# Kernel optimization log

Hardware: AMD Instinct MI355X
Metric: run time of the kernel (lower is better)

## Reference

```python
import jax, jax.numpy as jnp
import numpy as np

B, T, D, U = 64, 512, 1024, 128


def setup_inputs() -> dict:
    key = jax.random.key(0)
    k1, k2, k3, k4, k5 = jax.random.split(key, 5)
    x = jax.random.normal(k1, (B, T, D), dtype=jnp.float32)
    mask = jnp.ones((B, T), dtype=jnp.int32)
    # learned parameters (glorot-ish scale for kernel)
    kernel = jax.random.normal(k2, (D, U), dtype=jnp.float32) * (1.0 / np.sqrt(D))
    bias = jnp.zeros((U,), dtype=jnp.float32)
    left_boundary = jax.random.normal(k3, (U,), dtype=jnp.float32) * 0.1
    right_boundary = jax.random.normal(k4, (U,), dtype=jnp.float32) * 0.1
    return {"x": x, "mask": mask, "kernel": kernel, "bias": bias,
            "left_boundary": left_boundary, "right_boundary": right_boundary}


def _shift_right(m):  # [B,T,1] -> pad one zero step at front along time
    return jnp.concatenate([jnp.zeros_like(m[:, :1]), m[:, :-1]], axis=1)


def _shift_left(m):  # [B,T,1] -> pad one zero step at end along time
    return jnp.concatenate([m[:, 1:], jnp.zeros_like(m[:, :1])], axis=1)


def reference(x, mask, kernel, bias, left_boundary, right_boundary):
    # input energy: linear activation of dense projection  [B,T,U]
    energy = jnp.einsum('btd,du->btu', x, kernel) + bias
    # boundary energies with mask (faithful to source semantics)
    m = mask.astype(energy.dtype)[:, :, None]                     # [B,T,1]
    start_mask = (m > _shift_right(m)).astype(energy.dtype)       # first valid step
    end_mask = (_shift_left(m) > m).astype(energy.dtype)          # as written in source
    energy = energy + start_mask * left_boundary[None, None, :]
    energy = energy + end_mask * right_boundary[None, None, :]
    return energy
```

## Files before the change

kernel.cpp:

```cpp
#include <hip/hip_runtime.h>

#define TT 512
#define DD 1024
#define UU 128
#define MM 32768
#define BK 64
#define NCHUNK 16

typedef short short8 __attribute__((ext_vector_type(8)));
typedef float f32x4 __attribute__((ext_vector_type(4)));

__device__ __forceinline__ unsigned short f2bf(float f) {
    union { float f; unsigned u; } v; v.f = f;
    unsigned u = v.u;
    return (unsigned short)((u + 0x7fffu + ((u >> 16) & 1u)) >> 16);
}

__device__ __forceinline__ void glds16(const void* g, void* l) {
    __builtin_amdgcn_global_load_lds(
        (const __attribute__((address_space(1))) void*)g,
        (__attribute__((address_space(3))) void*)l, 16, 0, 0);
}

__global__ __launch_bounds__(256) void wprep_kernel(const float* __restrict__ w,
                                                    unsigned short* __restrict__ wt) {
    int tg = blockIdx.x * 256 + threadIdx.x;
    int kg = tg & 7;
    int n  = (tg >> 3) & 127;
    int kc = tg >> 10;
    union { unsigned short s[8]; uint4 v; } o;
#pragma unroll
    for (int j = 0; j < 8; ++j) {
        int k = kc * 64 + kg * 8 + j;
        o.s[j] = f2bf(w[k * 128 + n]);
    }
    *(uint4*)(wt + tg * 8) = o.v;
}

__global__ __launch_bounds__(256, 4) void crf_energy_kernel(
    const float* __restrict__ x,
    const int* __restrict__ mask,
    const unsigned short* __restrict__ wt,
    const float* __restrict__ bias,
    const float* __restrict__ lb,
    const float* __restrict__ rb,
    float* __restrict__ out)
{
    __shared__ float lAf[32 * 64];
    __shared__ unsigned short lBs[128 * 64];

    const int tid  = threadIdx.x;
    const int w    = tid >> 6;
    const int lane = tid & 63;
    const int q    = lane >> 4;
    const int r    = lane & 15;

    const int mt   = w >> 1;
    const int nh   = w & 1;
    const int row0 = blockIdx.x * 32;

    int a_m[2], a_g[2];
#pragma unroll
    for (int j = 0; j < 2; ++j) {
        a_m[j] = w * 8 + j * 4 + (lane >> 4);
        a_g[j] = (lane & 15) ^ (a_m[j] & 15);
    }
    int b_n[4], b_g[4];
#pragma unroll
    for (int j = 0; j < 4; ++j) {
        b_n[j] = w * 32 + j * 8 + (lane >> 3);
        b_g[j] = (lane & 7) ^ (b_n[j] & 7);
    }
    char* const lA_base = (char*)lAf + w * 2048;
    char* const lB_base = (char*)lBs + w * 4096;

    f32x4 acc[4];
#pragma unroll
    for (int nt = 0; nt < 4; ++nt) acc[nt] = (f32x4){0.f, 0.f, 0.f, 0.f};

    for (int kc = 0; kc < NCHUNK; ++kc) {
#pragma unroll
        for (int j = 0; j < 2; ++j)
            glds16(x + (size_t)(row0 + a_m[j]) * DD + kc * BK + a_g[j] * 4,
                   lA_base + j * 1024);
#pragma unroll
        for (int j = 0; j < 4; ++j)
            glds16(wt + (size_t)kc * 8192 + b_n[j] * 64 + b_g[j] * 8,
                   lB_base + j * 1024);
        __syncthreads();

#pragma unroll
        for (int ks = 0; ks < 2; ++ks) {
            const int m  = mt * 16 + r;
            const int g0 = ks * 8 + q * 2;
            const float4 lo = *(const float4*)(&lAf[m * 64 + ((g0     ^ (m & 15)) * 4)]);
            const float4 hi = *(const float4*)(&lAf[m * 64 + (((g0+1) ^ (m & 15)) * 4)]);
            union { unsigned short s[8]; short8 v; } pk;
            pk.s[0] = f2bf(lo.x); pk.s[1] = f2bf(lo.y);
            pk.s[2] = f2bf(lo.z); pk.s[3] = f2bf(lo.w);
            pk.s[4] = f2bf(hi.x); pk.s[5] = f2bf(hi.y);
            pk.s[6] = f2bf(hi.z); pk.s[7] = f2bf(hi.w);
            const short8 a = pk.v;

            short8 b[4];
            const int gb = ks * 4 + q;
#pragma unroll
            for (int nt = 0; nt < 4; ++nt) {
                const int n = nh * 64 + nt * 16 + r;
                b[nt] = *(const short8*)(&lBs[n * 64 + ((gb ^ (n & 7)) * 8)]);
            }
#pragma unroll
            for (int nt = 0; nt < 4; ++nt)
                acc[nt] = __builtin_amdgcn_mfma_f32_16x16x32_bf16(a, b[nt], acc[nt], 0, 0, 0);
        }
        __syncthreads();
    }

#pragma unroll
    for (int reg = 0; reg < 4; ++reg) {
        const int m = row0 + mt * 16 + q * 4 + reg;
        const int t = m & (TT - 1);
        const int cur  = mask[m];
        const int prev = (t != 0)      ? mask[m - 1] : 0;
        const int nxt  = (t != TT - 1) ? mask[m + 1] : 0;
        const float sm = (cur > prev) ? 1.f : 0.f;
        const float em = (nxt > cur)  ? 1.f : 0.f;
#pragma unroll
        for (int nt = 0; nt < 4; ++nt) {
            const int n = nh * 64 + nt * 16 + r;
            float e = acc[nt][reg] + bias[n] + sm * lb[n] + em * rb[n];
            out[(size_t)m * UU + n] = e;
        }
    }
}

extern "C" void kernel_launch(void* const* d_in, const int* in_sizes, int n_in,
                              void* d_out, int out_size, void* d_ws, size_t ws_size,
                              hipStream_t stream) {
    const float* x    = (const float*)d_in[0];
    const int*   mask = (const int*)d_in[1];
    const float* w    = (const float*)d_in[2];
    const float* bias = (const float*)d_in[3];
    const float* lb   = (const float*)d_in[4];
    const float* rb   = (const float*)d_in[5];
    float* out = (float*)d_out;
    unsigned short* wt = (unsigned short*)d_ws;

    wprep_kernel<<<64, 256, 0, stream>>>(w, wt);
    crf_energy_kernel<<<1024, 256, 0, stream>>>(x, mask, wt, bias, lb, rb, out);
}
```

Before: 214.8 us.

## Double-buffer LDS tiles and double the row tile per block

```diff
diff --git a/kernel.cpp b/kernel.cpp
--- a/kernel.cpp
+++ b/kernel.cpp
@@ -37,7 +37,7 @@
     *(uint4*)(wt + tg * 8) = o.v;
 }
 
-__global__ __launch_bounds__(256, 4) void crf_energy_kernel(
+__global__ __launch_bounds__(256, 2) void crf_energy_kernel(
     const float* __restrict__ x,
     const int* __restrict__ mask,
     const unsigned short* __restrict__ wt,
@@ -46,8 +46,8 @@
     const float* __restrict__ rb,
     float* __restrict__ out)
 {
-    __shared__ float lAf[32 * 64];
-    __shared__ unsigned short lBs[128 * 64];
+    __shared__ float lAf[2][64 * 64];
+    __shared__ unsigned short lBs[2][128 * 64];
 
     const int tid  = threadIdx.x;
     const int w    = tid >> 6;
@@ -55,14 +55,14 @@
     const int q    = lane >> 4;
     const int r    = lane & 15;
 
-    const int mt   = w >> 1;
+    const int mh   = w >> 1;
     const int nh   = w & 1;
-    const int row0 = blockIdx.x * 32;
+    const int row0 = blockIdx.x * 64;
 
-    int a_m[2], a_g[2];
+    int a_m[4], a_g[4];
 #pragma unroll
-    for (int j = 0; j < 2; ++j) {
-        a_m[j] = w * 8 + j * 4 + (lane >> 4);
+    for (int j = 0; j < 4; ++j) {
+        a_m[j] = w * 16 + j * 4 + (lane >> 4);
         a_g[j] = (lane & 15) ^ (a_m[j] & 15);
     }
     int b_n[4], b_g[4];
@@ -71,65 +71,91 @@
         b_n[j] = w * 32 + j * 8 + (lane >> 3);
         b_g[j] = (lane & 7) ^ (b_n[j] & 7);
     }
-    char* const lA_base = (char*)lAf + w * 2048;
-    char* const lB_base = (char*)lBs + w * 4096;
 
-    f32x4 acc[4];
+    f32x4 acc[2][4];
 #pragma unroll
-    for (int nt = 0; nt < 4; ++nt) acc[nt] = (f32x4){0.f, 0.f, 0.f, 0.f};
+    for (int mt = 0; mt < 2; ++mt)
+#pragma unroll
+        for (int nt = 0; nt < 4; ++nt) acc[mt][nt] = (f32x4){0.f, 0.f, 0.f, 0.f};
+
+#pragma unroll
+    for (int j = 0; j < 4; ++j)
+        glds16(x + (size_t)(row0 + a_m[j]) * DD + a_g[j] * 4,
+               (char*)lAf[0] + w * 4096 + j * 1024);
+#pragma unroll
+    for (int j = 0; j < 4; ++j)
+        glds16(wt + b_n[j] * 64 + b_g[j] * 8,
+               (char*)lBs[0] + w * 4096 + j * 1024);
+    __syncthreads();
 
     for (int kc = 0; kc < NCHUNK; ++kc) {
+        const int cb = kc & 1;
+
+        if (kc < NCHUNK - 1) {
+            const int pb = cb ^ 1;
 #pragma unroll
-        for (int j = 0; j < 2; ++j)
-            glds16(x + (size_t)(row0 + a_m[j]) * DD + kc * BK + a_g[j] * 4,
-                   lA_base + j * 1024);
+            for (int j = 0; j < 4; ++j)
+                glds16(x + (size_t)(row0 + a_m[j]) * DD + (kc + 1) * BK + a_g[j] * 4,
+                       (char*)lAf[pb] + w * 4096 + j * 1024);
 #pragma unroll
-        for (int j = 0; j < 4; ++j)
-            glds16(wt + (size_t)kc * 8192 + b_n[j] * 64 + b_g[j] * 8,
-                   lB_base + j * 1024);
-        __syncthreads();
+            for (int j = 0; j < 4; ++j)
+                glds16(wt + (size_t)(kc + 1) * 8192 + b_n[j] * 64 + b_g[j] * 8,
+                       (char*)lBs[pb] + w * 4096 + j * 1024);
+        }
 
+        const float* const lA = lAf[cb];
+        const unsigned short* const lB = lBs[cb];
 #pragma unroll
         for (int ks = 0; ks < 2; ++ks) {
-            const int m  = mt * 16 + r;
-            const int g0 = ks * 8 + q * 2;
-            const float4 lo = *(const float4*)(&lAf[m * 64 + ((g0     ^ (m & 15)) * 4)]);
-            const float4 hi = *(const float4*)(&lAf[m * 64 + (((g0+1) ^ (m & 15)) * 4)]);
-            union { unsigned short s[8]; short8 v; } pk;
-            pk.s[0] = f2bf(lo.x); pk.s[1] = f2bf(lo.y);
-            pk.s[2] = f2bf(lo.z); pk.s[3] = f2bf(lo.w);
-            pk.s[4] = f2bf(hi.x); pk.s[5] = f2bf(hi.y);
-            pk.s[6] = f2bf(hi.z); pk.s[7] = f2bf(hi.w);
-            const short8 a = pk.v;
-
+            short8 a[2];
+#pragma unroll
+            for (int mt = 0; mt < 2; ++mt) {
+                const int m  = mh * 32 + mt * 16 + r;
+                const int g0 = ks * 8 + q * 2;
+                const float4 lo = *(const float4*)(&lA[m * 64 + (((g0    ) ^ (m & 15)) * 4)]);
+                const float4 hi = *(const float4*)(&lA[m * 64 + (((g0 + 1) ^ (m & 15)) * 4)]);
+                union { unsigned short s[8]; short8 v; } pk;
+                pk.s[0] = f2bf(lo.x); pk.s[1] = f2bf(lo.y);
+                pk.s[2] = f2bf(lo.z); pk.s[3] = f2bf(lo.w);
+                pk.s[4] = f2bf(hi.x); pk.s[5] = f2bf(hi.y);
+                pk.s[6] = f2bf(hi.z); pk.s[7] = f2bf(hi.w);
+                a[mt] = pk.v;
+            }
             short8 b[4];
             const int gb = ks * 4 + q;
 #pragma unroll
             for (int nt = 0; nt < 4; ++nt) {
                 const int n = nh * 64 + nt * 16 + r;
-                b[nt] = *(const short8*)(&lBs[n * 64 + ((gb ^ (n & 7)) * 8)]);
+                b[nt] = *(const short8*)(&lB[n * 64 + ((gb ^ (n & 7)) * 8)]);
             }
 #pragma unroll
-            for (int nt = 0; nt < 4; ++nt)
-                acc[nt] = __builtin_amdgcn_mfma_f32_16x16x32_bf16(a, b[nt], acc[nt], 0, 0, 0);
+            for (int mt = 0; mt < 2; ++mt)
+#pragma unroll
+                for (int nt = 0; nt < 4; ++nt)
+                    acc[mt][nt] = __builtin_amdgcn_mfma_f32_16x16x32_bf16(
+                        a[mt], b[nt], acc[mt][nt], 0, 0, 0);
         }
+
         __syncthreads();
     }
 
 #pragma unroll
-    for (int reg = 0; reg < 4; ++reg) {
-        const int m = row0 + mt * 16 + q * 4 + reg;
-        const int t = m & (TT - 1);
-        const int cur  = mask[m];
-        const int prev = (t != 0)      ? mask[m - 1] : 0;
-        const int nxt  = (t != TT - 1) ? mask[m + 1] : 0;
-        const float sm = (cur > prev) ? 1.f : 0.f;
-        const float em = (nxt > cur)  ? 1.f : 0.f;
+    for (int mt = 0; mt < 2; ++mt) {
 #pragma unroll
-        for (int nt = 0; nt < 4; ++nt) {
-            const int n = nh * 64 + nt * 16 + r;
-            float e = acc[nt][reg] + bias[n] + sm * lb[n] + em * rb[n];
-            out[(size_t)m * UU + n] = e;
+        for (int reg = 0; reg < 4; ++reg) {
+            const int m = row0 + mh * 32 + mt * 16 + q * 4 + reg;
+            const int t = m & (TT - 1);
+            const int cur  = mask[m];
+            const int prev = (t != 0)      ? mask[m - 1] : 0;
+            const int nxt  = (t != TT - 1) ? mask[m + 1] : 0;
+            const float sm = (cur > prev) ? 1.f : 0.f;
+            const float em = (nxt > cur)  ? 1.f : 0.f;
+#pragma unroll
+            for (int nt = 0; nt < 4; ++nt) {
+                const int n = nh * 64 + nt * 16 + r;
+                float e = acc[mt][nt][reg] + bias[n] + sm * lb[n] + em * rb[n];
+                out[(size_t)m * UU + n] = e;
+            }
         }
     }
 }
@@ -147,5 +173,5 @@
     unsigned short* wt = (unsigned short*)d_ws;
 
     wprep_kernel<<<64, 256, 0, stream>>>(w, wt);
-    crf_energy_kernel<<<1024, 256, 0, stream>>>(x, mask, wt, bias, lb, rb, out);
+    crf_energy_kernel<<<512, 256, 0, stream>>>(x, mask, wt, bias, lb, rb, out);
 }
```

Result: no change. 214.6 us (-0.1%).

## Triple-buffer LDS tiles with async prefetch two chunks ahead

Applied to the files above, without the earlier changes.

```diff
diff --git a/kernel.cpp b/kernel.cpp
--- a/kernel.cpp
+++ b/kernel.cpp
@@ -6,6 +6,7 @@
 #define MM 32768
 #define BK 64
 #define NCHUNK 16
+#define NBUF 3
 
 typedef short short8 __attribute__((ext_vector_type(8)));
 typedef float f32x4 __attribute__((ext_vector_type(4)));
@@ -37,7 +38,7 @@
     *(uint4*)(wt + tg * 8) = o.v;
 }
 
-__global__ __launch_bounds__(256, 4) void crf_energy_kernel(
+__global__ __launch_bounds__(256, 2) void crf_energy_kernel(
     const float* __restrict__ x,
     const int* __restrict__ mask,
     const unsigned short* __restrict__ wt,
@@ -46,8 +47,8 @@
     const float* __restrict__ rb,
     float* __restrict__ out)
 {
-    __shared__ float lAf[32 * 64];
-    __shared__ unsigned short lBs[128 * 64];
+    __shared__ float lAf[NBUF][32 * 64];
+    __shared__ unsigned short lBs[NBUF][128 * 64];
 
     const int tid  = threadIdx.x;
     const int w    = tid >> 6;
@@ -71,30 +72,42 @@
         b_n[j] = w * 32 + j * 8 + (lane >> 3);
         b_g[j] = (lane & 7) ^ (b_n[j] & 7);
     }
-    char* const lA_base = (char*)lAf + w * 2048;
-    char* const lB_base = (char*)lBs + w * 4096;
+
+    auto stage = [&](int kc, int buf) {
+#pragma unroll
+        for (int j = 0; j < 2; ++j)
+            glds16(x + (size_t)(row0 + a_m[j]) * DD + kc * BK + a_g[j] * 4,
+                   (char*)lAf[buf] + w * 2048 + j * 1024);
+#pragma unroll
+        for (int j = 0; j < 4; ++j)
+            glds16(wt + (size_t)kc * 8192 + b_n[j] * 64 + b_g[j] * 8,
+                   (char*)lBs[buf] + w * 4096 + j * 1024);
+    };
 
     f32x4 acc[4];
 #pragma unroll
     for (int nt = 0; nt < 4; ++nt) acc[nt] = (f32x4){0.f, 0.f, 0.f, 0.f};
 
+    stage(0, 0);
+    stage(1, 1);
+
     for (int kc = 0; kc < NCHUNK; ++kc) {
-#pragma unroll
-        for (int j = 0; j < 2; ++j)
-            glds16(x + (size_t)(row0 + a_m[j]) * DD + kc * BK + a_g[j] * 4,
-                   lA_base + j * 1024);
-#pragma unroll
-        for (int j = 0; j < 4; ++j)
-            glds16(wt + (size_t)kc * 8192 + b_n[j] * 64 + b_g[j] * 8,
-                   lB_base + j * 1024);
-        __syncthreads();
+        if (kc < NCHUNK - 1) {
+            asm volatile("s_waitcnt vmcnt(6)\n\ts_barrier" ::: "memory");
+        } else {
+            asm volatile("s_waitcnt vmcnt(0)\n\ts_barrier" ::: "memory");
+        }
 
+        if (kc + 2 < NCHUNK) stage(kc + 2, (kc + 2) % NBUF);
+
+        const float* const lA = lAf[kc % NBUF];
+        const unsigned short* const lB = lBs[kc % NBUF];
 #pragma unroll
         for (int ks = 0; ks < 2; ++ks) {
             const int m  = mt * 16 + r;
             const int g0 = ks * 8 + q * 2;
-            const float4 lo = *(const float4*)(&lAf[m * 64 + ((g0     ^ (m & 15)) * 4)]);
-            const float4 hi = *(const float4*)(&lAf[m * 64 + (((g0+1) ^ (m & 15)) * 4)]);
+            const float4 lo = *(const float4*)(&lA[m * 64 + (((g0    ) ^ (m & 15)) * 4)]);
+            const float4 hi = *(const float4*)(&lA[m * 64 + (((g0 + 1) ^ (m & 15)) * 4)]);
             union { unsigned short s[8]; short8 v; } pk;
             pk.s[0] = f2bf(lo.x); pk.s[1] = f2bf(lo.y);
             pk.s[2] = f2bf(lo.z); pk.s[3] = f2bf(lo.w);
@@ -107,13 +120,12 @@
 #pragma unroll
             for (int nt = 0; nt < 4; ++nt) {
                 const int n = nh * 64 + nt * 16 + r;
-                b[nt] = *(const short8*)(&lBs[n * 64 + ((gb ^ (n & 7)) * 8)]);
+                b[nt] = *(const short8*)(&lB[n * 64 + ((gb ^ (n & 7)) * 8)]);
             }
 #pragma unroll
             for (int nt = 0; nt < 4; ++nt)
                 acc[nt] = __builtin_amdgcn_mfma_f32_16x16x32_bf16(a, b[nt], acc[nt], 0, 0, 0);
         }
-        __syncthreads();
     }
 
 #pragma unroll
```

Measured after the change: 215.1 us. No clear change (+0.1%).
